# Optimization experiments

Hardware: AMD Instinct MI355X
Metric: run time of the kernel (lower is better)

## Reference

```python
import jax, jax.numpy as jnp
import numpy as np

HIDDEN = 2048
IN = 2
OUT = 2
T = 1024


def setup_inputs() -> dict:
    key = jax.random.key(0)
    ks = jax.random.split(key, 8)
    s_ih = 1.0 / np.sqrt(HIDDEN)
    return {
        "features": jax.random.normal(ks[0], (1, HIDDEN), dtype=jnp.float32),
        "point_cloud": jax.random.normal(ks[1], (1, T, IN), dtype=jnp.float32),
        "W_ih": jax.random.uniform(ks[2], (4 * HIDDEN, IN), jnp.float32, -s_ih, s_ih),
        "W_hh": jax.random.uniform(ks[3], (4 * HIDDEN, HIDDEN), jnp.float32, -s_ih, s_ih),
        "b_ih": jax.random.uniform(ks[4], (4 * HIDDEN,), jnp.float32, -s_ih, s_ih),
        "b_hh": jax.random.uniform(ks[5], (4 * HIDDEN,), jnp.float32, -s_ih, s_ih),
        "W_fc": jax.random.uniform(ks[6], (OUT, HIDDEN), jnp.float32, -s_ih, s_ih),
        "b_fc": jax.random.uniform(ks[7], (OUT,), jnp.float32, -s_ih, s_ih),
        "max_seq_len": T,
    }


def reference(features, point_cloud, W_ih, W_hh, b_ih, b_hh, W_fc, b_fc, max_seq_len):
    # Training branch of DecoderRNN.forward: teacher-forced LSTMCell decode.
    H = features.shape[1]
    c0 = jnp.zeros_like(features)  # [B, H]

    def step(carry, x_t):
        h, c = carry
        gates = x_t @ W_ih.T + b_ih + h @ W_hh.T + b_hh  # [B, 4H]
        i, f, g, o = jnp.split(gates, 4, axis=-1)  # PyTorch LSTMCell gate order
        c_new = jax.nn.sigmoid(f) * c + jax.nn.sigmoid(i) * jnp.tanh(g)
        h_new = jax.nn.sigmoid(o) * jnp.tanh(c_new)
        out = h_new @ W_fc.T + b_fc  # [B, OUT]
        return (h_new, c_new), out

    xs = jnp.swapaxes(point_cloud, 0, 1)  # [T, B, IN]
    _, outs = jax.lax.scan(step, (features, c0), xs)  # outs: [T, B, OUT]
    # original returns outputs[:, 1:, :] which drops the initial zeros row
    return jnp.swapaxes(outs, 0, 1)  # [B, T, OUT]
```

## Files before the change

kernel.cpp:

```cpp
#include <hip/hip_runtime.h>
#include <math.h>
#include <stdint.h>

#define HIDDEN 2048
#define TSTEPS 1024
#define NWG 256
#define TPB 512
#define UPW 8
#define CPT 16
#define FLAG_STRIDE 32
#define GO_STRIDE 32

__device__ __forceinline__ float sigmoidf_(float x) { return 1.0f / (1.0f + __expf(-x)); }

__global__ __launch_bounds__(TPB, 2)
void lstm_v10(const float* __restrict__ features,
              const float* __restrict__ pc,
              const float* __restrict__ W_ih,
              const float* __restrict__ W_hh,
              const float* __restrict__ b_ih,
              const float* __restrict__ b_hh,
              const float* __restrict__ W_fc,
              const float* __restrict__ b_fc,
              float* __restrict__ out,
              int*   __restrict__ flags,
              int*   __restrict__ go,
              float* __restrict__ hhist)
{
    const int b    = blockIdx.x;
    const int t    = threadIdx.x;
    const int lane = t & 63;
    const int wave = t >> 6;
    const int g    = t & 3;
    const int cc   = t >> 2;
    const int col0 = cc * CPT;
    const bool isw255 = (b == NWG - 1);

    __builtin_amdgcn_fence(__ATOMIC_ACQUIRE, "agent");

    __shared__ float pc_sh[2 * TSTEPS];
    __shared__ float red[8 * 32];
    __shared__ float outred[16];
    __shared__ int   ls_go;

    if (t == 0) ls_go = 0;

    {
        const float4* p4 = reinterpret_cast<const float4*>(pc);
        reinterpret_cast<float4*>(pc_sh)[t] = p4[t];
    }

    float w[UPW][CPT];
    {
        const int baserow = g * HIDDEN + b * UPW;
        #pragma unroll
        for (int ji = 0; ji < UPW; ++ji) {
            const float4* src = reinterpret_cast<const float4*>(
                W_hh + (size_t)(baserow + ji) * HIDDEN + col0);
            float4 a0 = src[0], a1 = src[1], a2 = src[2], a3 = src[3];
            w[ji][0]  = a0.x; w[ji][1]  = a0.y; w[ji][2]  = a0.z; w[ji][3]  = a0.w;
            w[ji][4]  = a1.x; w[ji][5]  = a1.y; w[ji][6]  = a1.z; w[ji][7]  = a1.w;
            w[ji][8]  = a2.x; w[ji][9]  = a2.y; w[ji][10] = a2.z; w[ji][11] = a2.w;
            w[ji][12] = a3.x; w[ji][13] = a3.y; w[ji][14] = a3.z; w[ji][15] = a3.w;
        }
    }

    float bias_r = 0.0f, wi0_r = 0.0f, wi1_r = 0.0f, creg = 0.0f;
    if (wave == 0) {
        const int l   = lane & 31;
        const int row = (l >> 3) * HIDDEN + b * UPW + (l & 7);
        bias_r = b_ih[row] + b_hh[row];
        wi0_r  = W_ih[row * 2 + 0];
        wi1_r  = W_ih[row * 2 + 1];
    }
    __syncthreads();

    const int* gop = go + (size_t)(b >> 2) * GO_STRIDE;

    for (int s = 0; s < TSTEPS; ++s) {
        const int rot = (s >= 1) && (b == ((s - 1) & 255));

        float hr[CPT];
        if (s == 0) {
            #pragma unroll
            for (int k = 0; k < CPT; k += 4) {
                float4 hv = *reinterpret_cast<const float4*>(features + col0 + k);
                hr[k] = hv.x; hr[k + 1] = hv.y; hr[k + 2] = hv.z; hr[k + 3] = hv.w;
            }
        } else {
            if (isw255) {
                while (__hip_atomic_load(&ls_go, __ATOMIC_RELAXED,
                                         __HIP_MEMORY_SCOPE_WORKGROUP) < s) {}
            } else {
                while (__hip_atomic_load(gop, __ATOMIC_RELAXED,
                                         __HIP_MEMORY_SCOPE_AGENT) < s) {}
            }
            const float* hsrc = hhist + (size_t)s * HIDDEN;
            #pragma unroll
            for (int k = 0; k < CPT; k += 4) {
                float4 hv = *reinterpret_cast<const float4*>(hsrc + col0 + k);
                hr[k] = hv.x; hr[k + 1] = hv.y; hr[k + 2] = hv.z; hr[k + 3] = hv.w;
            }
        }

        float acc[UPW];
        #pragma unroll
        for (int ji = 0; ji < UPW; ++ji) acc[ji] = 0.0f;
        #pragma unroll
        for (int k = 0; k < CPT; ++k) {
            #pragma unroll
            for (int ji = 0; ji < UPW; ++ji) acc[ji] += w[ji][k] * hr[k];
        }
        #pragma unroll
        for (int m = 4; m < 64; m <<= 1) {
            #pragma unroll
            for (int ji = 0; ji < UPW; ++ji) acc[ji] += __shfl_xor(acc[ji], m);
        }
        if (lane < 4) {
            #pragma unroll
            for (int ji = 0; ji < UPW; ++ji) red[wave * 32 + lane * 8 + ji] = acc[ji];
        }

        if (rot) {
            float po0 = 0.0f, po1 = 0.0f;
            #pragma unroll
            for (int k = 0; k < CPT; ++k) {
                po0 += hr[k] * W_fc[col0 + k];
                po1 += hr[k] * W_fc[HIDDEN + col0 + k];
            }
            #pragma unroll
            for (int m = 1; m < 64; m <<= 1) {
                po0 += __shfl_xor(po0, m);
                po1 += __shfl_xor(po1, m);
            }
            if (lane == 0) { outred[wave * 2 + 0] = po0; outred[wave * 2 + 1] = po1; }
        }
        __syncthreads();

        if (wave == 0) {
            const int l = lane & 31;
            float sum = 0.0f;
            #pragma unroll
            for (int ww = 0; ww < 8; ++ww) sum += red[ww * 32 + l];
            const float x0 = pc_sh[2 * s], x1 = pc_sh[2 * s + 1];
            const float gate = sum + bias_r + wi0_r * x0 + wi1_r * x1;
            const float iv = __shfl(gate, (lane & 7));
            const float fv = __shfl(gate, 8 + (lane & 7));
            const float gv = __shfl(gate, 16 + (lane & 7));
            const float ov = __shfl(gate, 24 + (lane & 7));
            const float cnew = sigmoidf_(fv) * creg + sigmoidf_(iv) * tanhf(gv);
            const float hnew = sigmoidf_(ov) * tanhf(cnew);
            creg = cnew;
            const uint32_t hb = __float_as_uint(hnew);

            const uint32_t lo = __shfl(hb, 2 * (lane & 3));
            const uint32_t hi = __shfl(hb, 2 * (lane & 3) + 1);
            if (lane < 4) {
                const uint64_t qv = (uint64_t)lo | ((uint64_t)hi << 32);
                uint64_t* dst = reinterpret_cast<uint64_t*>(
                    hhist + (size_t)(s + 1) * HIDDEN + b * UPW) + lane;
                __hip_atomic_store(dst, qv, __ATOMIC_RELAXED, __HIP_MEMORY_SCOPE_AGENT);
            }
            asm volatile("s_waitcnt vmcnt(0)" ::: "memory");
            if (lane == 0) {
                __hip_atomic_store(flags + (size_t)b * FLAG_STRIDE, s + 1,
                                   __ATOMIC_RELAXED, __HIP_MEMORY_SCOPE_AGENT);
            }
        }

        if (isw255 && wave == 7) {
            const int l4 = lane * 4;
            const int* f0p = flags + (size_t)(l4 + 0) * FLAG_STRIDE;
            const int* f1p = flags + (size_t)(l4 + 1) * FLAG_STRIDE;
            const int* f2p = flags + (size_t)(l4 + 2) * FLAG_STRIDE;
            const int* f3p = flags + (size_t)(l4 + 3) * FLAG_STRIDE;
            for (;;) {
                const int f0 = __hip_atomic_load(f0p, __ATOMIC_RELAXED, __HIP_MEMORY_SCOPE_AGENT);
                const int f1 = __hip_atomic_load(f1p, __ATOMIC_RELAXED, __HIP_MEMORY_SCOPE_AGENT);
                const int f2 = __hip_atomic_load(f2p, __ATOMIC_RELAXED, __HIP_MEMORY_SCOPE_AGENT);
                const int f3 = __hip_atomic_load(f3p, __ATOMIC_RELAXED, __HIP_MEMORY_SCOPE_AGENT);
                const bool ok = (f0 >= s + 1) & (f1 >= s + 1) & (f2 >= s + 1) & (f3 >= s + 1);
                if (__all(ok)) break;
            }
            __hip_atomic_store(go + (size_t)lane * GO_STRIDE, s + 1,
                               __ATOMIC_RELAXED, __HIP_MEMORY_SCOPE_AGENT);
            if (lane == 0) {
                __hip_atomic_store(&ls_go, s + 1, __ATOMIC_RELAXED,
                                   __HIP_MEMORY_SCOPE_WORKGROUP);
            }
        }

        if (rot && t == 64) {
            float o0 = 0.0f, o1 = 0.0f;
            #pragma unroll
            for (int ww = 0; ww < 8; ++ww) { o0 += outred[ww * 2]; o1 += outred[ww * 2 + 1]; }
            out[(s - 1) * 2 + 0] = 0.25f * o0 + b_fc[0];
            out[(s - 1) * 2 + 1] = 0.25f * o1 + b_fc[1];
        }
    }

    if (isw255) {
        while (__hip_atomic_load(&ls_go, __ATOMIC_RELAXED,
                                 __HIP_MEMORY_SCOPE_WORKGROUP) < TSTEPS) {}
        const float* hsrc = hhist + (size_t)TSTEPS * HIDDEN;
        float po0 = 0.0f, po1 = 0.0f;
        #pragma unroll
        for (int k = 0; k < CPT; ++k) {
            const float hv = hsrc[col0 + k];
            po0 += hv * W_fc[col0 + k];
            po1 += hv * W_fc[HIDDEN + col0 + k];
        }
        #pragma unroll
        for (int m = 1; m < 64; m <<= 1) {
            po0 += __shfl_xor(po0, m);
            po1 += __shfl_xor(po1, m);
        }
        if (lane == 0) { outred[wave * 2 + 0] = po0; outred[wave * 2 + 1] = po1; }
        __syncthreads();
        if (t == 0) {
            float o0 = 0.0f, o1 = 0.0f;
            #pragma unroll
            for (int ww = 0; ww < 8; ++ww) { o0 += outred[ww * 2]; o1 += outred[ww * 2 + 1]; }
            out[(TSTEPS - 1) * 2 + 0] = 0.25f * o0 + b_fc[0];
            out[(TSTEPS - 1) * 2 + 1] = 0.25f * o1 + b_fc[1];
        }
    }
}

extern "C" void kernel_launch(void* const* d_in, const int* in_sizes, int n_in,
                              void* d_out, int out_size, void* d_ws, size_t ws_size,
                              hipStream_t stream) {
    const float* features = (const float*)d_in[0];
    const float* pc       = (const float*)d_in[1];
    const float* W_ih     = (const float*)d_in[2];
    const float* W_hh     = (const float*)d_in[3];
    const float* b_ih     = (const float*)d_in[4];
    const float* b_hh     = (const float*)d_in[5];
    const float* W_fc     = (const float*)d_in[6];
    const float* b_fc     = (const float*)d_in[7];
    float* out = (float*)d_out;

    const size_t flags_bytes = (size_t)NWG * FLAG_STRIDE * sizeof(int);
    const size_t go_bytes    = (size_t)64 * GO_STRIDE * sizeof(int);
    const size_t hh_off      = flags_bytes + go_bytes;

    int*   flags = (int*)d_ws;
    int*   go    = (int*)((char*)d_ws + flags_bytes);
    float* hhist = (float*)((char*)d_ws + hh_off);

    hipMemsetAsync(d_ws, 0, hh_off, stream);

    hipLaunchKernelGGL(lstm_v10, dim3(NWG), dim3(TPB), 0, stream,
                       features, pc, W_ih, W_hh, b_ih, b_hh, W_fc, b_fc,
                       out, flags, go, hhist);
}
```

Before: 3.614 ms.

## Add per-XCD relay workgroup for L2-local go signal in grid barrier

At startup, one workgroup per XCD is elected through a compare-exchange on a workspace slot. Each step, that workgroup polls all 256 flags and writes a per-XCD local go counter with sc0 stores. The other workgroups spin on this local counter with sc0 loads, which can be served from the XCD's own L2, and fall back to the global go counter every few polls. The aim is to cut the cross-XCD latency of the per-timestep barrier. In exchange, each step now has more workgroups polling the flags, and correctness depends on how the cache-coherence modifiers behave.

```diff
diff --git a/kernel.cpp b/kernel.cpp
--- a/kernel.cpp
+++ b/kernel.cpp
@@ -10,11 +10,23 @@
 #define CPT 16
 #define FLAG_STRIDE 32
 #define GO_STRIDE 32
+#define NXCD 8
 
 __device__ __forceinline__ float sigmoidf_(float x) { return 1.0f / (1.0f + __expf(-x)); }
 
+__device__ __forceinline__ int load_sc0(const int* p) {
+    int v;
+    asm volatile("global_load_dword %0, %1, off sc0\n\t"
+                 "s_waitcnt vmcnt(0)"
+                 : "=v"(v) : "v"(p) : "memory");
+    return v;
+}
+__device__ __forceinline__ void store_sc0(int* p, int v) {
+    asm volatile("global_store_dword %0, %1, off sc0" :: "v"(p), "v"(v) : "memory");
+}
+
 __global__ __launch_bounds__(TPB, 2)
-void lstm_v10(const float* __restrict__ features,
+void lstm_v11(const float* __restrict__ features,
               const float* __restrict__ pc,
               const float* __restrict__ W_ih,
               const float* __restrict__ W_hh,
@@ -25,6 +37,8 @@
               float* __restrict__ out,
               int*   __restrict__ flags,
               int*   __restrict__ go,
+              int*   __restrict__ elect,
+              int*   __restrict__ go_local,
               float* __restrict__ hhist)
 {
     const int b    = blockIdx.x;
@@ -38,12 +52,28 @@
 
     __builtin_amdgcn_fence(__ATOMIC_ACQUIRE, "agent");
 
+    uint32_t xcdreg;
+    asm volatile("s_getreg_b32 %0, hwreg(HW_REG_XCC_ID)" : "=s"(xcdreg));
+    const int myxcd = (int)(xcdreg & (NXCD - 1));
+
     __shared__ float pc_sh[2 * TSTEPS];
     __shared__ float red[8 * 32];
     __shared__ float outred[16];
     __shared__ int   ls_go;
-
-    if (t == 0) ls_go = 0;
+    __shared__ int   ls_relay;
+
+    if (t == 0) {
+        ls_go = 0;
+        int won = 0;
+        if (!isw255) {
+            int expected = 0;
+            won = __hip_atomic_compare_exchange_strong(
+                      elect + (size_t)myxcd * GO_STRIDE, &expected, 1,
+                      __ATOMIC_RELAXED, __ATOMIC_RELAXED, __HIP_MEMORY_SCOPE_AGENT)
+                      ? 1 : 0;
+        }
+        ls_relay = won;
+    }
 
     {
         const float4* p4 = reinterpret_cast<const float4*>(pc);
@@ -74,8 +104,11 @@
         wi1_r  = W_ih[row * 2 + 1];
     }
     __syncthreads();
+    const bool relaywg = (ls_relay != 0);
 
     const int* gop = go + (size_t)(b >> 2) * GO_STRIDE;
+    const int* lgp = go_local + (size_t)myxcd * GO_STRIDE;
+    int*       lgs = go_local + (size_t)myxcd * GO_STRIDE;
 
     for (int s = 0; s < TSTEPS; ++s) {
         const int rot = (s >= 1) && (b == ((s - 1) & 255));
@@ -92,8 +125,13 @@
                 while (__hip_atomic_load(&ls_go, __ATOMIC_RELAXED,
                                          __HIP_MEMORY_SCOPE_WORKGROUP) < s) {}
             } else {
-                while (__hip_atomic_load(gop, __ATOMIC_RELAXED,
-                                         __HIP_MEMORY_SCOPE_AGENT) < s) {}
+                for (;;) {
+                    if (load_sc0(lgp) >= s) break;
+                    if (load_sc0(lgp) >= s) break;
+                    if (load_sc0(lgp) >= s) break;
+                    if (__hip_atomic_load(gop, __ATOMIC_RELAXED,
+                                          __HIP_MEMORY_SCOPE_AGENT) >= s) break;
+                }
             }
             const float* hsrc = hhist + (size_t)s * HIDDEN;
             #pragma unroll
@@ -190,6 +228,23 @@
             }
         }
 
+        if (relaywg && wave == 7) {
+            const int l4 = lane * 4;
+            const int* f0p = flags + (size_t)(l4 + 0) * FLAG_STRIDE;
+            const int* f1p = flags + (size_t)(l4 + 1) * FLAG_STRIDE;
+            const int* f2p = flags + (size_t)(l4 + 2) * FLAG_STRIDE;
+            const int* f3p = flags + (size_t)(l4 + 3) * FLAG_STRIDE;
+            for (;;) {
+                const int f0 = __hip_atomic_load(f0p, __ATOMIC_RELAXED, __HIP_MEMORY_SCOPE_AGENT);
+                const int f1 = __hip_atomic_load(f1p, __ATOMIC_RELAXED, __HIP_MEMORY_SCOPE_AGENT);
+                const int f2 = __hip_atomic_load(f2p, __ATOMIC_RELAXED, __HIP_MEMORY_SCOPE_AGENT);
+                const int f3 = __hip_atomic_load(f3p, __ATOMIC_RELAXED, __HIP_MEMORY_SCOPE_AGENT);
+                const bool ok = (f0 >= s + 1) & (f1 >= s + 1) & (f2 >= s + 1) & (f3 >= s + 1);
+                if (__all(ok)) break;
+            }
+            if (lane == 0) store_sc0(lgs, s + 1);
+        }
+
         if (rot && t == 64) {
             float o0 = 0.0f, o1 = 0.0f;
             #pragma unroll
@@ -242,15 +297,19 @@
 
     const size_t flags_bytes = (size_t)NWG * FLAG_STRIDE * sizeof(int);
     const size_t go_bytes    = (size_t)64 * GO_STRIDE * sizeof(int);
-    const size_t hh_off      = flags_bytes + go_bytes;
+    const size_t elect_bytes = (size_t)NXCD * GO_STRIDE * sizeof(int);
+    const size_t gol_bytes   = (size_t)NXCD * GO_STRIDE * sizeof(int);
+    const size_t hdr_bytes   = 65536;
 
     int*   flags = (int*)d_ws;
     int*   go    = (int*)((char*)d_ws + flags_bytes);
-    float* hhist = (float*)((char*)d_ws + hh_off);
-
-    hipMemsetAsync(d_ws, 0, hh_off, stream);
-
-    hipLaunchKernelGGL(lstm_v10, dim3(NWG), dim3(TPB), 0, stream,
+    int*   elect = (int*)((char*)d_ws + flags_bytes + go_bytes);
+    int*   go_l  = (int*)((char*)d_ws + flags_bytes + go_bytes + elect_bytes);
+    float* hhist = (float*)((char*)d_ws + hdr_bytes);
+
+    hipMemsetAsync(d_ws, 0, flags_bytes + go_bytes + elect_bytes + gol_bytes, stream);
+
+    hipLaunchKernelGGL(lstm_v11, dim3(NWG), dim3(TPB), 0, stream,
                        features, pc, W_ih, W_hh, b_ih, b_hh, W_fc, b_fc,
-                       out, flags, go, hhist);
+                       out, flags, go, elect, go_l, hhist);
 }
```

Result: slower. 3.715 ms (+2.8%).

## Replace two-level flag/go barrier with packed byte flags polled by every workgroup

Applied to the files above, without the earlier changes.

The two-hop grid barrier is removed. Before, workgroup 255 gathered 256 padded int flags and then broadcast go counters. Now each workgroup writes a one-byte step counter (mod 256) into a packed 256-byte array, and wave 7 of every workgroup polls the whole array with 32 64-bit loads, using a byte-wise nonzero test that accepts step s or s+1. This takes one global round trip off each step's critical path, at the cost of heavier contention on a single shared cache line set and reliance on byte atomics wrapping safely.

```diff
diff --git a/kernel.cpp b/kernel.cpp
--- a/kernel.cpp
+++ b/kernel.cpp
@@ -8,13 +8,18 @@
 #define TPB 512
 #define UPW 8
 #define CPT 16
-#define FLAG_STRIDE 32
-#define GO_STRIDE 32
 
 __device__ __forceinline__ float sigmoidf_(float x) { return 1.0f / (1.0f + __expf(-x)); }
 
+__device__ __forceinline__ uint64_t nzbytes(uint64_t x) {
+    uint64_t t = (x | (x >> 4)) & 0x0F0F0F0F0F0F0F0FULL;
+    t = (t | (t >> 2)) & 0x0303030303030303ULL;
+    t = (t | (t >> 1)) & 0x0101010101010101ULL;
+    return t;
+}
+
 __global__ __launch_bounds__(TPB, 2)
-void lstm_v10(const float* __restrict__ features,
+void lstm_v12(const float* __restrict__ features,
               const float* __restrict__ pc,
               const float* __restrict__ W_ih,
               const float* __restrict__ W_hh,
@@ -23,9 +28,8 @@
               const float* __restrict__ W_fc,
               const float* __restrict__ b_fc,
               float* __restrict__ out,
-              int*   __restrict__ flags,
-              int*   __restrict__ go,
-              float* __restrict__ hhist)
+              uint8_t* __restrict__ flags8,
+              float*   __restrict__ hhist)
 {
     const int b    = blockIdx.x;
     const int t    = threadIdx.x;
@@ -34,7 +38,6 @@
     const int g    = t & 3;
     const int cc   = t >> 2;
     const int col0 = cc * CPT;
-    const bool isw255 = (b == NWG - 1);
 
     __builtin_amdgcn_fence(__ATOMIC_ACQUIRE, "agent");
 
@@ -75,27 +78,38 @@
     }
     __syncthreads();
 
-    const int* gop = go + (size_t)(b >> 2) * GO_STRIDE;
+    const uint64_t* fq = reinterpret_cast<const uint64_t*>(flags8);
+    const uint64_t  k1 = 0x0101010101010101ULL;
 
     for (int s = 0; s < TSTEPS; ++s) {
         const int rot = (s >= 1) && (b == ((s - 1) & 255));
 
-        float hr[CPT];
-        if (s == 0) {
-            #pragma unroll
-            for (int k = 0; k < CPT; k += 4) {
-                float4 hv = *reinterpret_cast<const float4*>(features + col0 + k);
-                hr[k] = hv.x; hr[k + 1] = hv.y; hr[k + 2] = hv.z; hr[k + 3] = hv.w;
-            }
-        } else {
-            if (isw255) {
+        if (s >= 1) {
+            if (wave == 7) {
+                const uint64_t e0 = k1 * (uint64_t)(s & 255);
+                const uint64_t e1 = k1 * (uint64_t)((s + 1) & 255);
+                for (;;) {
+                    uint64_t q = e0;
+                    if (lane < 32) {
+                        q = __hip_atomic_load(fq + lane, __ATOMIC_RELAXED,
+                                              __HIP_MEMORY_SCOPE_AGENT);
+                    }
+                    const uint64_t bad = nzbytes(q ^ e0) & nzbytes(q ^ e1);
+                    if (__all(bad == 0)) break;
+                }
+                if (lane == 0) {
+                    __hip_atomic_store(&ls_go, s, __ATOMIC_RELAXED,
+                                       __HIP_MEMORY_SCOPE_WORKGROUP);
+                }
+            } else {
                 while (__hip_atomic_load(&ls_go, __ATOMIC_RELAXED,
                                          __HIP_MEMORY_SCOPE_WORKGROUP) < s) {}
-            } else {
-                while (__hip_atomic_load(gop, __ATOMIC_RELAXED,
-                                         __HIP_MEMORY_SCOPE_AGENT) < s) {}
-            }
-            const float* hsrc = hhist + (size_t)s * HIDDEN;
+            }
+        }
+
+        float hr[CPT];
+        {
+            const float* hsrc = (s == 0) ? features : (hhist + (size_t)s * HIDDEN);
             #pragma unroll
             for (int k = 0; k < CPT; k += 4) {
                 float4 hv = *reinterpret_cast<const float4*>(hsrc + col0 + k);
@@ -163,30 +177,8 @@
             }
             asm volatile("s_waitcnt vmcnt(0)" ::: "memory");
             if (lane == 0) {
-                __hip_atomic_store(flags + (size_t)b * FLAG_STRIDE, s + 1,
+                __hip_atomic_store(flags8 + b, (uint8_t)((s + 1) & 255),
                                    __ATOMIC_RELAXED, __HIP_MEMORY_SCOPE_AGENT);
-            }
-        }
-
-        if (isw255 && wave == 7) {
-            const int l4 = lane * 4;
-            const int* f0p = flags + (size_t)(l4 + 0) * FLAG_STRIDE;
-            const int* f1p = flags + (size_t)(l4 + 1) * FLAG_STRIDE;
-            const int* f2p = flags + (size_t)(l4 + 2) * FLAG_STRIDE;
-            const int* f3p = flags + (size_t)(l4 + 3) * FLAG_STRIDE;
-            for (;;) {
-                const int f0 = __hip_atomic_load(f0p, __ATOMIC_RELAXED, __HIP_MEMORY_SCOPE_AGENT);
-                const int f1 = __hip_atomic_load(f1p, __ATOMIC_RELAXED, __HIP_MEMORY_SCOPE_AGENT);
-                const int f2 = __hip_atomic_load(f2p, __ATOMIC_RELAXED, __HIP_MEMORY_SCOPE_AGENT);
-                const int f3 = __hip_atomic_load(f3p, __ATOMIC_RELAXED, __HIP_MEMORY_SCOPE_AGENT);
-                const bool ok = (f0 >= s + 1) & (f1 >= s + 1) & (f2 >= s + 1) & (f3 >= s + 1);
-                if (__all(ok)) break;
-            }
-            __hip_atomic_store(go + (size_t)lane * GO_STRIDE, s + 1,
-                               __ATOMIC_RELAXED, __HIP_MEMORY_SCOPE_AGENT);
-            if (lane == 0) {
-                __hip_atomic_store(&ls_go, s + 1, __ATOMIC_RELAXED,
-                                   __HIP_MEMORY_SCOPE_WORKGROUP);
             }
         }
 
@@ -199,9 +191,28 @@
         }
     }
 
-    if (isw255) {
-        while (__hip_atomic_load(&ls_go, __ATOMIC_RELAXED,
-                                 __HIP_MEMORY_SCOPE_WORKGROUP) < TSTEPS) {}
+    if (b == NWG - 1) {
+        if (wave == 7) {
+            const uint64_t e0 = k1 * (uint64_t)(TSTEPS & 255);
+            const uint64_t e1 = k1 * (uint64_t)((TSTEPS + 1) & 255);
+            for (;;) {
+                uint64_t q = e0;
+                if (lane < 32) {
+                    q = __hip_atomic_load(fq + lane, __ATOMIC_RELAXED,
+                                          __HIP_MEMORY_SCOPE_AGENT);
+                }
+                const uint64_t bad = nzbytes(q ^ e0) & nzbytes(q ^ e1);
+                if (__all(bad == 0)) break;
+            }
+            if (lane == 0) {
+                __hip_atomic_store(&ls_go, TSTEPS, __ATOMIC_RELAXED,
+                                   __HIP_MEMORY_SCOPE_WORKGROUP);
+            }
+        } else {
+            while (__hip_atomic_load(&ls_go, __ATOMIC_RELAXED,
+                                     __HIP_MEMORY_SCOPE_WORKGROUP) < TSTEPS) {}
+        }
+
         const float* hsrc = hhist + (size_t)TSTEPS * HIDDEN;
         float po0 = 0.0f, po1 = 0.0f;
         #pragma unroll
@@ -240,17 +251,12 @@
     const float* b_fc     = (const float*)d_in[7];
     float* out = (float*)d_out;
 
-    const size_t flags_bytes = (size_t)NWG * FLAG_STRIDE * sizeof(int);
-    const size_t go_bytes    = (size_t)64 * GO_STRIDE * sizeof(int);
-    const size_t hh_off      = flags_bytes + go_bytes;
-
-    int*   flags = (int*)d_ws;
-    int*   go    = (int*)((char*)d_ws + flags_bytes);
-    float* hhist = (float*)((char*)d_ws + hh_off);
-
-    hipMemsetAsync(d_ws, 0, hh_off, stream);
-
-    hipLaunchKernelGGL(lstm_v10, dim3(NWG), dim3(TPB), 0, stream,
+    uint8_t* flags8 = (uint8_t*)d_ws;
+    float*   hhist  = (float*)((char*)d_ws + 4096);
+
+    hipMemsetAsync(d_ws, 0, 4096, stream);
+
+    hipLaunchKernelGGL(lstm_v12, dim3(NWG), dim3(TPB), 0, stream,
                        features, pc, W_ih, W_hh, b_ih, b_hh, W_fc, b_fc,
-                       out, flags, go, hhist);
+                       out, flags8, hhist);
 }
```

Result: slower. 9.185 ms (+154.2%).

## Poll global go flag from one wave and broadcast via LDS; move output reduction into wave 0

Applied to the files above, without the earlier changes.

Only wave 7 of each workgroup now spins on the global go counter and republishes the step through an LDS flag; the other waves spin on that LDS flag instead of hammering global memory. The per-step output projection's final reduction is moved into wave 0 after the flag store, taking it off the critical path of the separate t==64 thread. Wave 0's partial is written and summed directly. This adds an extra LDS hop of latency on the wake-up path and relies on outred from other waves being visible without a barrier.

```diff
diff --git a/kernel.cpp b/kernel.cpp
--- a/kernel.cpp
+++ b/kernel.cpp
@@ -14,7 +14,7 @@
 __device__ __forceinline__ float sigmoidf_(float x) { return 1.0f / (1.0f + __expf(-x)); }
 
 __global__ __launch_bounds__(TPB, 2)
-void lstm_v10(const float* __restrict__ features,
+void lstm_v13(const float* __restrict__ features,
               const float* __restrict__ pc,
               const float* __restrict__ W_ih,
               const float* __restrict__ W_hh,
@@ -80,22 +80,26 @@
     for (int s = 0; s < TSTEPS; ++s) {
         const int rot = (s >= 1) && (b == ((s - 1) & 255));
 
-        float hr[CPT];
-        if (s == 0) {
-            #pragma unroll
-            for (int k = 0; k < CPT; k += 4) {
-                float4 hv = *reinterpret_cast<const float4*>(features + col0 + k);
-                hr[k] = hv.x; hr[k + 1] = hv.y; hr[k + 2] = hv.z; hr[k + 3] = hv.w;
-            }
-        } else {
+        if (s >= 1) {
             if (isw255) {
                 while (__hip_atomic_load(&ls_go, __ATOMIC_RELAXED,
                                          __HIP_MEMORY_SCOPE_WORKGROUP) < s) {}
-            } else {
+            } else if (wave == 7) {
                 while (__hip_atomic_load(gop, __ATOMIC_RELAXED,
                                          __HIP_MEMORY_SCOPE_AGENT) < s) {}
-            }
-            const float* hsrc = hhist + (size_t)s * HIDDEN;
+                if (lane == 0) {
+                    __hip_atomic_store(&ls_go, s, __ATOMIC_RELAXED,
+                                       __HIP_MEMORY_SCOPE_WORKGROUP);
+                }
+            } else {
+                while (__hip_atomic_load(&ls_go, __ATOMIC_RELAXED,
+                                         __HIP_MEMORY_SCOPE_WORKGROUP) < s) {}
+            }
+        }
+
+        float hr[CPT];
+        {
+            const float* hsrc = (s == 0) ? features : (hhist + (size_t)s * HIDDEN);
             #pragma unroll
             for (int k = 0; k < CPT; k += 4) {
                 float4 hv = *reinterpret_cast<const float4*>(hsrc + col0 + k);
@@ -121,7 +125,7 @@
             for (int ji = 0; ji < UPW; ++ji) red[wave * 32 + lane * 8 + ji] = acc[ji];
         }
 
-        if (rot) {
+        if (rot && wave != 0) {
             float po0 = 0.0f, po1 = 0.0f;
             #pragma unroll
             for (int k = 0; k < CPT; ++k) {
@@ -165,6 +169,28 @@
             if (lane == 0) {
                 __hip_atomic_store(flags + (size_t)b * FLAG_STRIDE, s + 1,
                                    __ATOMIC_RELAXED, __HIP_MEMORY_SCOPE_AGENT);
+            }
+
+            if (rot) {
+                float po0 = 0.0f, po1 = 0.0f;
+                #pragma unroll
+                for (int k = 0; k < CPT; ++k) {
+                    po0 += hr[k] * W_fc[col0 + k];
+                    po1 += hr[k] * W_fc[HIDDEN + col0 + k];
+                }
+                #pragma unroll
+                for (int m = 1; m < 64; m <<= 1) {
+                    po0 += __shfl_xor(po0, m);
+                    po1 += __shfl_xor(po1, m);
+                }
+                if (lane == 0) {
+                    outred[0] = po0; outred[1] = po1;
+                    float o0 = 0.0f, o1 = 0.0f;
+                    #pragma unroll
+                    for (int ww = 0; ww < 8; ++ww) { o0 += outred[ww * 2]; o1 += outred[ww * 2 + 1]; }
+                    out[(s - 1) * 2 + 0] = 0.25f * o0 + b_fc[0];
+                    out[(s - 1) * 2 + 1] = 0.25f * o1 + b_fc[1];
+                }
             }
         }
 
@@ -189,14 +215,6 @@
                                    __HIP_MEMORY_SCOPE_WORKGROUP);
             }
         }
-
-        if (rot && t == 64) {
-            float o0 = 0.0f, o1 = 0.0f;
-            #pragma unroll
-            for (int ww = 0; ww < 8; ++ww) { o0 += outred[ww * 2]; o1 += outred[ww * 2 + 1]; }
-            out[(s - 1) * 2 + 0] = 0.25f * o0 + b_fc[0];
-            out[(s - 1) * 2 + 1] = 0.25f * o1 + b_fc[1];
-        }
     }
 
     if (isw255) {
@@ -250,7 +268,7 @@
 
     hipMemsetAsync(d_ws, 0, hh_off, stream);
 
-    hipLaunchKernelGGL(lstm_v10, dim3(NWG), dim3(TPB), 0, stream,
+    hipLaunchKernelGGL(lstm_v13, dim3(NWG), dim3(TPB), 0, stream,
                        features, pc, W_ih, W_hh, b_ih, b_hh, W_fc, b_fc,
                        out, flags, go, hhist);
 }
```

Result: no change. 3.600 ms (-0.4%).
